# Kernel optimization log

Hardware: AMD Instinct MI355X
Metric: run time of the kernel (lower is better)

## Reference

```python
import jax, jax.numpy as jnp
import numpy as np
from jax import lax

K2 = 3                 # support_kernel_size
TARGET_OCC = 0.5
OCC_W = 10.0
ITERS = 10             # flood-fill iterations
THRESH = 0.5
STEEP = 20.0

# 6-neighbor 3D cross kernel (plus-shaped), shape [O=1, I=1, 3, 3, 3]
_cross_np = np.zeros((1, 1, 3, 3, 3), dtype=np.float32)
for dz, dy, dx in [(0, 1, 1), (2, 1, 1), (1, 0, 1), (1, 2, 1), (1, 1, 0), (1, 1, 2)]:
    _cross_np[0, 0, dz, dy, dx] = 1.0


def _conv3d(x, k, pad):
    # x: [B, C, D, H, W], k: [O, I, kd, kh, kw]
    return lax.conv_general_dilated(
        x, k, window_strides=(1, 1, 1), padding=pad,
        dimension_numbers=('NCDHW', 'OIDHW', 'NCDHW'))


def setup_inputs() -> dict:
    key = jax.random.key(0)
    voxel_grid = jax.random.uniform(key, (4, 1, 128, 128, 128), dtype=jnp.float32)
    return {"voxel_grid": voxel_grid}


def reference(voxel_grid):
    B, C, D, H, W = voxel_grid.shape
    N = B * D * H * W
    dt = voxel_grid.dtype

    # ---- overhang score: vectorized over all z-slices at once ----
    # per-slice conv2d(3x3 ones) == conv3d with kernel depth 1
    k2 = jnp.ones((1, 1, 1, K2, K2), dt)
    below = voxel_grid[:, :, :-1]          # [B,1,D-1,H,W]
    curr = voxel_grid[:, :, 1:]
    below_support = _conv3d(below, k2, ((0, 0), (1, 1), (1, 1)))
    support_ratio = below_support / (K2 * K2)
    overhang = (curr * (1.0 - support_ratio)).sum() / N

    # ---- surface area score ----
    k3 = jnp.ones((1, 1, 3, 3, 3), dt)
    neighbor_solid = _conv3d(voxel_grid, k3, ((1, 1), (1, 1), (1, 1)))
    surface_term = neighbor_solid.sum() / 27.0 / N

    occupancy = voxel_grid.sum() / N
    occupancy_penalty = OCC_W * (occupancy - TARGET_OCC) ** 2

    # differentiable flood-fill (diff_find_enclosed_voids)
    seed = jnp.zeros_like(voxel_grid).at[:, :, 5, 5, 5].set(1.0)
    cross = jnp.asarray(_cross_np, dt)
    not_solid = 1.0 - voxel_grid

    def body(i, mask):
        c = _conv3d(mask, cross, ((1, 1), (1, 1), (1, 1)))
        act = jax.nn.sigmoid(STEEP * (c - THRESH))
        return jnp.maximum(mask, act) * not_solid

    enclosed = lax.fori_loop(0, ITERS, body, seed)
    resin_trap_penalty = 100.0 * enclosed.sum() / N

    surface_score = surface_term - resin_trap_penalty - occupancy_penalty
    return overhang, surface_score
```

## Files before the change

### kernel.cpp

```cpp
#include <hip/hip_runtime.h>

#define HW    (128*128)
#define DHW   (128*128*128)
#define NTOT  (4*DHW)
#define NBLK  1024
#define TOTB  (NBLK + 4)

__device__ __forceinline__ float sigf(float x){ return 1.0f/(1.0f+__expf(-x)); }
__device__ __forceinline__ float4 ld4(const float* p){ return *(const float4*)p; }

__global__ __launch_bounds__(256, 4) void mega_k(
    const float* __restrict__ v, float* __restrict__ p_occ,
    float* __restrict__ p_surf, float* __restrict__ p_over,
    float* __restrict__ p_trap)
{
    __shared__ float4 smem4[1445];
    __shared__ float sred[16];
    float* smem = (float*)smem4;

    const int bid = blockIdx.x;
    const int tid = threadIdx.x;
    const float4 zero4 = make_float4(0,0,0,0);

    if (bid < 4) {
        const int b = bid;
        const size_t gb = (size_t)b * DHW;
        const int ty = tid & 15, tz = tid >> 4;
        const float a_lo = sigf(-10.0f), a_hi = sigf(10.0f);
        #define M(zz,yy) (smem + (((zz)*17 + (yy))*20))

        float m[16], nv[16];
        {
            const float* rv = v + gb + ((size_t)tz*128 + ty)*128;
            int dzy = abs(tz-5) + abs(ty-5);
            #pragma unroll
            for (int q = 0; q < 4; ++q) {
                int x4 = 4*q;
                float4 a = ld4(rv + x4);
                nv[x4+0]=1.f-a.x; nv[x4+1]=1.f-a.y; nv[x4+2]=1.f-a.z; nv[x4+3]=1.f-a.w;
                int d0=dzy+abs(x4+0-5), d1=dzy+abs(x4+1-5);
                int d2=dzy+abs(x4+2-5), d3=dzy+abs(x4+3-5);
                m[x4+0] = ((d0==0)?1.f:((d0==1)?a_hi:a_lo)) * nv[x4+0];
                m[x4+1] = ((d1==0)?1.f:((d1==1)?a_hi:a_lo)) * nv[x4+1];
                m[x4+2] = ((d2==0)?1.f:((d2==1)?a_hi:a_lo)) * nv[x4+2];
                m[x4+3] = ((d3==0)?1.f:((d3==1)?a_hi:a_lo)) * nv[x4+3];
                *(float4*)(M(tz,ty) + x4) = make_float4(m[x4+0],m[x4+1],m[x4+2],m[x4+3]);
            }
        }
        const float xrE = a_lo * (1.f - v[gb + ((size_t)tz*128 + ty)*128 + 16]);
        {
            int a = tid >> 4, e = tid & 15;
            M(16,a)[e] = a_lo * (1.f - v[gb + ((size_t)16*128 + a)*128 + e]);
            M(a,16)[e] = a_lo * (1.f - v[gb + ((size_t)a*128 + 16)*128 + e]);
        }
        __syncthreads();

        for (int it = 0; it < 9; ++it) {
            const float* YM = M(tz,ty-1);
            const float* YP = M(tz,ty+1);
            const float* ZM = M(tz-1,ty);
            const float* ZP = M(tz+1,ty);
            float nm[16];
            #pragma unroll
            for (int q = 0; q < 4; ++q) {
                int x4 = 4*q;
                float4 ym = (ty > 0) ? *(const float4*)(YM + x4) : zero4;
                float4 yp = *(const float4*)(YP + x4);
                float4 zm = (tz > 0) ? *(const float4*)(ZM + x4) : zero4;
                float4 zp = *(const float4*)(ZP + x4);
                float xl = (q == 0) ? 0.f : m[x4-1];
                float xr = (q == 3) ? xrE : m[x4+4];
                float s0 = xl      + m[x4+1] + ym.x + yp.x + zm.x + zp.x;
                float s1 = m[x4+0] + m[x4+2] + ym.y + yp.y + zm.y + zp.y;
                float s2 = m[x4+1] + m[x4+3] + ym.z + yp.z + zm.z + zp.z;
                float s3 = m[x4+2] + xr      + ym.w + yp.w + zm.w + zp.w;
                nm[x4+0] = fmaxf(m[x4+0], sigf(20.f*s0 - 10.f)) * nv[x4+0];
                nm[x4+1] = fmaxf(m[x4+1], sigf(20.f*s1 - 10.f)) * nv[x4+1];
                nm[x4+2] = fmaxf(m[x4+2], sigf(20.f*s2 - 10.f)) * nv[x4+2];
                nm[x4+3] = fmaxf(m[x4+3], sigf(20.f*s3 - 10.f)) * nv[x4+3];
            }
            __syncthreads();
            float* W = M(tz,ty);
            #pragma unroll
            for (int q = 0; q < 4; ++q) {
                int x4 = 4*q;
                *(float4*)(W + x4) = make_float4(nm[x4+0],nm[x4+1],nm[x4+2],nm[x4+3]);
                m[x4+0]=nm[x4+0]; m[x4+1]=nm[x4+1]; m[x4+2]=nm[x4+2]; m[x4+3]=nm[x4+3];
            }
            __syncthreads();
        }

        float d = 0.f;
        #pragma unroll
        for (int x = 0; x < 16; ++x) d += m[x] - a_lo * nv[x];
        #pragma unroll
        for (int o = 32; o; o >>= 1) d += __shfl_down(d, o, 64);
        int lane = tid & 63, wid = tid >> 6;
        if (lane == 0) sred[wid] = d;
        __syncthreads();
        if (tid == 0) p_trap[b] = sred[0] + sred[1] + sred[2] + sred[3];
        #undef M
    } else {
        const int rid = bid - 4;
        const int b   = rid >> 8;
        const int rem = rid & 255;
        const int z0  = (rem >> 4) * 8;
        const int y0  = (rem & 15) * 8;
        const int tx  = tid & 31;
        const int tz  = tid >> 5;
        const int z   = z0 + tz;
        const int x4  = tx * 4;
        const size_t gb = (size_t)b * DHW;
        const float* cp = v + gb + (size_t)z * HW;
        const float* bp = cp - HW;

        float occ = 0.f, surf = 0.f, over = 0.f;

        auto xsum = [&](float4 q) -> float4 {
            float ql = __shfl_up(q.w, 1);   if (tx == 0)  ql = 0.f;
            float qr = __shfl_down(q.x, 1); if (tx == 31) qr = 0.f;
            return make_float4(ql+q.x+q.y, q.x+q.y+q.z, q.y+q.z+q.w, q.z+q.w+qr);
        };

        const float wz  = (z==0 || z==127) ? 2.f : 3.f;
        const float wx0 = (x4==0)   ? 2.f : 3.f;
        const float wx3 = (x4==124) ? 2.f : 3.f;
        const float inv9 = 1.f/9.f;
        const bool hasb = (z >= 1);

        float4 c_cur = ld4(cp + y0*128 + x4);
        float4 Pm = zero4, Pc = zero4;
        if (hasb) {
            float4 bm = (y0 >= 1) ? ld4(bp + (y0-1)*128 + x4) : zero4;
            float4 bc = ld4(bp + y0*128 + x4);
            Pm = xsum(bm);
            Pc = xsum(bc);
        }

        #pragma unroll
        for (int i = 0; i < 8; ++i) {
            const int y = y0 + i;
            float4 c_nxt = zero4;
            if (i < 7) c_nxt = ld4(cp + (y+1)*128 + x4);
            float4 bn = zero4;
            if (hasb) {
                int gy = y + 1;
                bn = (gy <= 127) ? ld4(bp + gy*128 + x4) : zero4;
            }
            float4 val = c_cur;
            occ += val.x + val.y + val.z + val.w;
            float wy = (y==0 || y==127) ? 2.f : 3.f;
            surf += wz*wy*(wx0*val.x + 3.f*val.y + 3.f*val.z + wx3*val.w);
            if (hasb) {
                float4 Pp = xsum(bn);
                float4 S = make_float4(Pm.x+Pc.x+Pp.x, Pm.y+Pc.y+Pp.y,
                                       Pm.z+Pc.z+Pp.z, Pm.w+Pc.w+Pp.w);
                over += val.x*(1.f - S.x*inv9) + val.y*(1.f - S.y*inv9)
                      + val.z*(1.f - S.z*inv9) + val.w*(1.f - S.w*inv9);
                Pm = Pc; Pc = Pp;
            }
            c_cur = c_nxt;
        }

        #pragma unroll
        for (int o = 32; o; o >>= 1) {
            occ  += __shfl_down(occ,  o, 64);
            surf += __shfl_down(surf, o, 64);
            over += __shfl_down(over, o, 64);
        }
        int lane = tid & 63, wid = tid >> 6;
        if (lane == 0) { sred[wid]=occ; sred[4+wid]=surf; sred[8+wid]=over; }
        __syncthreads();
        if (tid == 0) {
            p_occ [rid] = sred[0]+sred[1]+sred[2]+sred[3];
            p_surf[rid] = sred[4]+sred[5]+sred[6]+sred[7];
            p_over[rid] = sred[8]+sred[9]+sred[10]+sred[11];
        }
    }
}

__global__ __launch_bounds__(1024) void finalize_k(
    const float* __restrict__ p_occ, const float* __restrict__ p_surf,
    const float* __restrict__ p_over, const float* __restrict__ p_trap,
    float* __restrict__ out)
{
    double occ=0, surf=0, over=0;
    for (int i = threadIdx.x; i < NBLK; i += 1024) {
        occ += p_occ[i]; surf += p_surf[i]; over += p_over[i];
    }
    __shared__ double sm[3][16];
    #pragma unroll
    for (int o = 32; o; o >>= 1) {
        occ  += __shfl_down(occ,  o, 64);
        surf += __shfl_down(surf, o, 64);
        over += __shfl_down(over, o, 64);
    }
    int lane = threadIdx.x & 63, wid = threadIdx.x >> 6;
    if (lane == 0) { sm[0][wid]=occ; sm[1][wid]=surf; sm[2][wid]=over; }
    __syncthreads();
    if (threadIdx.x == 0) {
        double so=0, ss=0, sv=0;
        for (int w = 0; w < 16; ++w) { so+=sm[0][w]; ss+=sm[1][w]; sv+=sm[2][w]; }
        double dS = (double)p_trap[0] + p_trap[1] + p_trap[2] + p_trap[3];
        double a_lo = 1.0 / (1.0 + exp(10.0));
        double N = (double)NTOT;
        double trap_sum = a_lo * (N - so) + dS;
        double occupancy = so / N;
        double occ_pen = 10.0 * (occupancy - 0.5) * (occupancy - 0.5);
        out[0] = (float)(sv / N);
        out[1] = (float)(ss / 27.0 / N - 100.0 * trap_sum / N - occ_pen);
    }
}

extern "C" void kernel_launch(void* const* d_in, const int* in_sizes, int n_in,
                              void* d_out, int out_size, void* d_ws, size_t ws_size,
                              hipStream_t stream)
{
    const float* v = (const float*)d_in[0];
    float* out = (float*)d_out;
    float* ws = (float*)d_ws;

    float* p_occ  = ws;
    float* p_surf = p_occ  + NBLK;
    float* p_over = p_surf + NBLK;
    float* p_trap = p_over + NBLK;

    mega_k<<<TOTB, 256, 0, stream>>>(v, p_occ, p_surf, p_over, p_trap);
    finalize_k<<<1, 1024, 0, stream>>>(p_occ, p_surf, p_over, p_trap, out);
}
```

Measured before the change: 84.46 us.

## Halve per-block row tile and issue all stencil loads upfront

Doubles the number of stencil blocks by shrinking each block's y-tile from 8 rows to 4, and replaces the rolling software-pipelined loop with all ten row loads issued at the start followed by straight-line compute. The aim is more memory-level parallelism and more blocks to spread across CUs, so this bandwidth-bound pass hides latency better. In exchange, the halo rows in the slice below are re-read proportionally more often, and more partial sums must be written and reduced. The flood-fill blocks, which likely dominate runtime, are left unchanged.

```diff
diff --git a/kernel.cpp b/kernel.cpp
--- a/kernel.cpp
+++ b/kernel.cpp
@@ -3,7 +3,7 @@
 #define HW    (128*128)
 #define DHW   (128*128*128)
 #define NTOT  (4*DHW)
-#define NBLK  1024
+#define NBLK  2048
 #define TOTB  (NBLK + 4)
 
 __device__ __forceinline__ float sigf(float x){ return 1.0f/(1.0f+__expf(-x)); }
@@ -102,10 +102,10 @@
         #undef M
     } else {
         const int rid = bid - 4;
-        const int b   = rid >> 8;
-        const int rem = rid & 255;
-        const int z0  = (rem >> 4) * 8;
-        const int y0  = (rem & 15) * 8;
+        const int b   = rid >> 9;
+        const int rem = rid & 511;
+        const int z0  = (rem >> 5) * 8;
+        const int y0  = (rem & 31) * 4;
         const int tx  = tid & 31;
         const int tz  = tid >> 5;
         const int z   = z0 + tz;
@@ -113,8 +113,22 @@
         const size_t gb = (size_t)b * DHW;
         const float* cp = v + gb + (size_t)z * HW;
         const float* bp = cp - HW;
-
-        float occ = 0.f, surf = 0.f, over = 0.f;
+        const bool hasb = (z >= 1);
+
+        float4 qc0 = ld4(cp + (y0+0)*128 + x4);
+        float4 qc1 = ld4(cp + (y0+1)*128 + x4);
+        float4 qc2 = ld4(cp + (y0+2)*128 + x4);
+        float4 qc3 = ld4(cp + (y0+3)*128 + x4);
+        float4 qb0 = zero4, qb1 = zero4, qb2 = zero4,
+               qb3 = zero4, qb4 = zero4, qb5 = zero4;
+        if (hasb) {
+            if (y0 >= 1)   qb0 = ld4(bp + (y0-1)*128 + x4);
+            qb1 = ld4(bp + (y0+0)*128 + x4);
+            qb2 = ld4(bp + (y0+1)*128 + x4);
+            qb3 = ld4(bp + (y0+2)*128 + x4);
+            qb4 = ld4(bp + (y0+3)*128 + x4);
+            if (y0+4 <= 127) qb5 = ld4(bp + (y0+4)*128 + x4);
+        }
 
         auto xsum = [&](float4 q) -> float4 {
             float ql = __shfl_up(q.w, 1);   if (tx == 0)  ql = 0.f;
@@ -122,45 +136,37 @@
             return make_float4(ql+q.x+q.y, q.x+q.y+q.z, q.y+q.z+q.w, q.z+q.w+qr);
         };
 
+        float occ = 0.f, surf = 0.f, over = 0.f;
         const float wz  = (z==0 || z==127) ? 2.f : 3.f;
         const float wx0 = (x4==0)   ? 2.f : 3.f;
         const float wx3 = (x4==124) ? 2.f : 3.f;
         const float inv9 = 1.f/9.f;
-        const bool hasb = (z >= 1);
-
-        float4 c_cur = ld4(cp + y0*128 + x4);
-        float4 Pm = zero4, Pc = zero4;
+
+        float4 P0 = zero4, P1 = zero4, P2 = zero4, P3 = zero4,
+               P4 = zero4, P5 = zero4;
         if (hasb) {
-            float4 bm = (y0 >= 1) ? ld4(bp + (y0-1)*128 + x4) : zero4;
-            float4 bc = ld4(bp + y0*128 + x4);
-            Pm = xsum(bm);
-            Pc = xsum(bc);
-        }
-
-        #pragma unroll
-        for (int i = 0; i < 8; ++i) {
-            const int y = y0 + i;
-            float4 c_nxt = zero4;
-            if (i < 7) c_nxt = ld4(cp + (y+1)*128 + x4);
-            float4 bn = zero4;
-            if (hasb) {
-                int gy = y + 1;
-                bn = (gy <= 127) ? ld4(bp + gy*128 + x4) : zero4;
-            }
-            float4 val = c_cur;
-            occ += val.x + val.y + val.z + val.w;
-            float wy = (y==0 || y==127) ? 2.f : 3.f;
-            surf += wz*wy*(wx0*val.x + 3.f*val.y + 3.f*val.z + wx3*val.w);
-            if (hasb) {
-                float4 Pp = xsum(bn);
-                float4 S = make_float4(Pm.x+Pc.x+Pp.x, Pm.y+Pc.y+Pp.y,
-                                       Pm.z+Pc.z+Pp.z, Pm.w+Pc.w+Pp.w);
-                over += val.x*(1.f - S.x*inv9) + val.y*(1.f - S.y*inv9)
-                      + val.z*(1.f - S.z*inv9) + val.w*(1.f - S.w*inv9);
-                Pm = Pc; Pc = Pp;
-            }
-            c_cur = c_nxt;
-        }
+            P0 = xsum(qb0); P1 = xsum(qb1); P2 = xsum(qb2);
+            P3 = xsum(qb3); P4 = xsum(qb4); P5 = xsum(qb5);
+        }
+
+        #define ROW(i, VAL, PA, PB, PC)                                        \
+        {                                                                      \
+            const int y = y0 + (i);                                            \
+            occ += VAL.x + VAL.y + VAL.z + VAL.w;                              \
+            float wy = (y==0 || y==127) ? 2.f : 3.f;                           \
+            surf += wz*wy*(wx0*VAL.x + 3.f*VAL.y + 3.f*VAL.z + wx3*VAL.w);     \
+            if (hasb) {                                                        \
+                float4 S = make_float4(PA.x+PB.x+PC.x, PA.y+PB.y+PC.y,         \
+                                       PA.z+PB.z+PC.z, PA.w+PB.w+PC.w);        \
+                over += VAL.x*(1.f - S.x*inv9) + VAL.y*(1.f - S.y*inv9)        \
+                      + VAL.z*(1.f - S.z*inv9) + VAL.w*(1.f - S.w*inv9);       \
+            }                                                                  \
+        }
+        ROW(0, qc0, P0, P1, P2)
+        ROW(1, qc1, P1, P2, P3)
+        ROW(2, qc2, P2, P3, P4)
+        ROW(3, qc3, P3, P4, P5)
+        #undef ROW
 
         #pragma unroll
         for (int o = 32; o; o >>= 1) {
```

After: 83.92 us (median of 2 runs). About the same (-0.6%).
